# Performance work log

Measured on AMD Instinct MI355X. Metric: run time of the kernel, lower is better.

## Reference

```python
import jax, jax.numpy as jnp
import numpy as np

ATTN_DIM = 512
LEN_DIM = 2048
HEAD = 8
RANK = 8
A_H = ATTN_DIM // HEAD      # 64
L_R = LEN_DIM // RANK       # 256
BS = 32


def setup_inputs() -> dict:
    key = jax.random.key(0)
    ks = jax.random.split(key, 8)
    s = 1.0 / np.sqrt(ATTN_DIM)
    return {
        "x": jax.random.normal(ks[0], (BS, LEN_DIM, ATTN_DIM), dtype=jnp.float32),
        "Wq": jax.random.normal(ks[1], (ATTN_DIM, ATTN_DIM), dtype=jnp.float32) * s,
        "bq": jax.random.normal(ks[2], (ATTN_DIM,), dtype=jnp.float32) * s,
        "Wk": jax.random.normal(ks[3], (ATTN_DIM, ATTN_DIM), dtype=jnp.float32) * s,
        "bk": jax.random.normal(ks[4], (ATTN_DIM,), dtype=jnp.float32) * s,
        "Wv": jax.random.normal(ks[5], (ATTN_DIM, ATTN_DIM), dtype=jnp.float32) * s,
        "bv": jax.random.normal(ks[6], (ATTN_DIM,), dtype=jnp.float32) * s,
        # xavier_normal-ish init for factor [1, a_h, l_r, rank]
        "factor": jax.random.normal(ks[7], (1, A_H, L_R, RANK), dtype=jnp.float32)
        * np.float32(np.sqrt(2.0 / (L_R + RANK))),
    }


def reference(x, Wq, bq, Wk, bk, Wv, bv, factor):
    bs = x.shape[0]
    hr = HEAD * RANK  # 64
    # projections (torch Linear: x @ W.T + b), then view to [bs, a_h, head*rank, l_r]
    q = (jnp.einsum("bld,ed->ble", x, Wq) + bq).reshape(bs, A_H, hr, L_R)
    k = (jnp.einsum("bld,ed->ble", x, Wk) + bk).reshape(bs, A_H, hr, L_R)
    v = (jnp.einsum("bld,ed->ble", x, Wv) + bv).reshape(bs, A_H, hr, L_R)
    f = factor[0]  # [a_h, l_r, rank]
    k = jnp.einsum("bahl,alr->bahr", k, f)  # [bs, a_h, hr, rank]
    v = jnp.einsum("bahl,alr->bahr", v, f)  # [bs, a_h, hr, rank]
    # scores = q^T @ k / sqrt(head*rank): [bs, a_h, l_r, rank]
    scores = jnp.einsum("bahl,bahr->balr", q, k) / jnp.sqrt(jnp.float32(hr))
    attn = jax.nn.softmax(scores, axis=-1)
    # attn @ v^T: [bs, a_h, l_r, hr]
    out = jnp.einsum("balr,bahr->balh", attn, v)
    return out.reshape(bs, LEN_DIM, ATTN_DIM)
```

## Files before the change

kernel.cpp:

```cpp
#include <hip/hip_runtime.h>
#include <hip/hip_bf16.h>
#include <stdint.h>


typedef unsigned short ushort_t;

using bf16x8 = __attribute__((ext_vector_type(8))) short;
using f32x4  = __attribute__((ext_vector_type(4))) float;

__device__ __forceinline__ float bf2f(unsigned short u) {
  union { unsigned int i; float f; } v;
  v.i = ((unsigned int)u) << 16;
  return v.f;
}
__device__ __forceinline__ unsigned short f2bf(float f) {
  __hip_bfloat16 h = __float2bfloat16(f);
  return *reinterpret_cast<unsigned short*>(&h);
}

__device__ __forceinline__ void load_lds16(const void* g, void* l) {
  __builtin_amdgcn_global_load_lds(
      (const __attribute__((address_space(1))) unsigned int*)g,
      (__attribute__((address_space(3))) unsigned int*)l,
      16, 0, 0);
}

__global__ __launch_bounds__(256)
void cast_f32_bf16(const float* __restrict__ src, ushort_t* __restrict__ dst,
                   int n4) {
  int i = blockIdx.x * blockDim.x + threadIdx.x;
  if (i < n4) {
    float4 v = ((const float4*)src)[i];
    ushort_t p[4] = {f2bf(v.x), f2bf(v.y), f2bf(v.z), f2bf(v.w)};
    *(uint2*)(dst + 4 * (size_t)i) = *(const uint2*)p;
  }
}

__global__ __launch_bounds__(256)
void wkv2_pre(const float* __restrict__ Wk, const float* __restrict__ bk,
              const float* __restrict__ Wv, const float* __restrict__ bv,
              const float* __restrict__ F,
              ushort_t* __restrict__ Wk2b, ushort_t* __restrict__ Wv2b,
              float* __restrict__ bk2g, float* __restrict__ bv2g) {
  const int a  = blockIdx.x;
  const int kv = blockIdx.y;
  const float* W = kv ? Wv : Wk;
  const float* B = kv ? bv : bk;
  ushort_t* Wo = kv ? Wv2b : Wk2b;
  float* bo = kv ? bv2g : bk2g;
  const int t = threadIdx.x;

  __shared__ float fs[256][8];
  {
    const float* Fp = F + (size_t)a * 2048 + (size_t)t * 8;
    *(float4*)&fs[t][0] = *(const float4*)Fp;
    *(float4*)&fs[t][4] = *(const float4*)(Fp + 4);
  }
  __syncthreads();

  for (int dblk = 0; dblk < 2; ++dblk) {
    const int d = dblk * 256 + t;
    float acc[2][8];
#pragma unroll
    for (int p = 0; p < 2; ++p)
#pragma unroll
      for (int r = 0; r < 8; ++r) acc[p][r] = 0.f;

    for (int lr = 0; lr < 256; ++lr) {
      const float w0 = W[(size_t)lr * 512 + d];
      const float w1 = W[(size_t)(256 + lr) * 512 + d];
      float4 fa = *(const float4*)&fs[lr][0];
      float4 fb = *(const float4*)&fs[lr][4];
      acc[0][0] += w0 * fa.x; acc[0][1] += w0 * fa.y;
      acc[0][2] += w0 * fa.z; acc[0][3] += w0 * fa.w;
      acc[0][4] += w0 * fb.x; acc[0][5] += w0 * fb.y;
      acc[0][6] += w0 * fb.z; acc[0][7] += w0 * fb.w;
      acc[1][0] += w1 * fa.x; acc[1][1] += w1 * fa.y;
      acc[1][2] += w1 * fa.z; acc[1][3] += w1 * fa.w;
      acc[1][4] += w1 * fb.x; acc[1][5] += w1 * fb.y;
      acc[1][6] += w1 * fb.z; acc[1][7] += w1 * fb.w;
    }
#pragma unroll
    for (int p = 0; p < 2; ++p)
#pragma unroll
      for (int r = 0; r < 8; ++r)
        Wo[((size_t)(a * 2 + p) * 8 + r) * 512 + d] = f2bf(acc[p][r]);
  }

  if (t < 16) {
    const int p = t >> 3, r = t & 7;
    float s = 0.f;
    for (int lr = 0; lr < 256; ++lr) s += B[p * 256 + lr] * fs[lr][r];
    bo[a * 16 + t] = s;
  }
}

__global__ __launch_bounds__(256)
void gemm_q(const ushort_t* __restrict__ X, const ushort_t* __restrict__ W,
            const float* __restrict__ Bi, ushort_t* __restrict__ O) {
  __shared__ __align__(16) short sA[128 * 64];
  __shared__ __align__(16) short sB[128 * 64];

  const int fid = blockIdx.x + 4 * blockIdx.y;
  const int swz = (fid & 7) * 256 + (fid >> 3);
  const int by  = swz >> 2;
  const int bx  = swz & 3;

  const int tid  = threadIdx.x;
  const int lane = tid & 63;
  const int wid  = tid >> 6;
  const int m0 = by * 128;
  const int n0 = bx * 128;
  const int wave_m = (wid & 1) * 64;
  const int wave_n = (wid >> 1) * 64;
  const int quad = lane >> 4;
  const int l15  = lane & 15;

  f32x4 acc[4][4];
#pragma unroll
  for (int i = 0; i < 4; ++i)
#pragma unroll
    for (int j = 0; j < 4; ++j) acc[i][j] = f32x4{0.f, 0.f, 0.f, 0.f};

  int srow[4], scol[4];
#pragma unroll
  for (int q = 0; q < 4; ++q) {
    const int c = q * 256 + wid * 64 + lane;
    srow[q] = c >> 3;
    scol[q] = ((c & 7) ^ ((c >> 3) & 7)) * 8;
  }

  for (int kt = 0; kt < 512; kt += 64) {
#pragma unroll
    for (int q = 0; q < 4; ++q) {
      const ushort_t* ga = X + ((size_t)(m0 + srow[q]) << 9) + kt + scol[q];
      const ushort_t* gb = W + ((size_t)(n0 + srow[q]) << 9) + kt + scol[q];
      load_lds16(ga, &sA[(q * 256 + wid * 64) * 8]);
      load_lds16(gb, &sB[(q * 256 + wid * 64) * 8]);
    }
    __syncthreads();

#pragma unroll
    for (int ks = 0; ks < 2; ++ks) {
      bf16x8 af[4], bfr[4];
#pragma unroll
      for (int i = 0; i < 4; ++i) {
        const int row = wave_m + i * 16 + l15;
        af[i] = *(const bf16x8*)&sA[row * 64 + ((ks * 4 + quad) ^ (row & 7)) * 8];
      }
#pragma unroll
      for (int j = 0; j < 4; ++j) {
        const int row = wave_n + j * 16 + l15;
        bfr[j] = *(const bf16x8*)&sB[row * 64 + ((ks * 4 + quad) ^ (row & 7)) * 8];
      }
#pragma unroll
      for (int i = 0; i < 4; ++i)
#pragma unroll
        for (int j = 0; j < 4; ++j)
          acc[i][j] = __builtin_amdgcn_mfma_f32_16x16x32_bf16(af[i], bfr[j],
                                                              acc[i][j], 0, 0, 0);
    }
    __syncthreads();
  }

#pragma unroll
  for (int j = 0; j < 4; ++j) {
    const int gn = n0 + wave_n + j * 16 + l15;
    const float bv = Bi[gn];
#pragma unroll
    for (int i = 0; i < 4; ++i) {
      const int gmBase = m0 + wave_m + i * 16 + quad * 4;
      f32x4 c = acc[i][j];
#pragma unroll
      for (int rg = 0; rg < 4; ++rg) {
        O[((size_t)(gmBase + rg) << 9) + gn] = f2bf(c[rg] + bv);
      }
    }
  }
}

__global__ __launch_bounds__(256)
void k2v2_gemm(const ushort_t* __restrict__ X,
               const ushort_t* __restrict__ Wk2b,
               const ushort_t* __restrict__ Wv2b,
               const float* __restrict__ bk2g, const float* __restrict__ bv2g,
               float* __restrict__ k2g, float* __restrict__ v2g) {
  const int a = blockIdx.x;
  const int b = blockIdx.y;
  __shared__ __align__(16) short sX[32 * 512];
  __shared__ __align__(16) short sW[32 * 512];

  const int t = threadIdx.x;
  const int lane = t & 63;
  const int wid  = t >> 6;

#pragma unroll
  for (int q = 0; q < 8; ++q) {
    const int c = q * 256 + wid * 64 + lane;
    const int row = c >> 6;
    const int sch = (c & 63) ^ (row & 7);
    const ushort_t* gx =
        X + ((size_t)(b * 2048 + a * 32 + row) << 9) + sch * 8;
    const ushort_t* gw =
        (row < 16 ? Wk2b + (size_t)(a * 16 + row) * 512
                  : Wv2b + (size_t)(a * 16 + row - 16) * 512) + sch * 8;
    load_lds16(gx, &sX[(q * 256 + wid * 64) * 8]);
    load_lds16(gw, &sW[(q * 256 + wid * 64) * 8]);
  }
  __syncthreads();

  const int kv = wid >> 1;
  const int mf = wid & 1;
  const int quad = lane >> 4;
  const int l15  = lane & 15;

  f32x4 acc = f32x4{0.f, 0.f, 0.f, 0.f};
  const int arow = mf * 16 + l15;
  const int brow = kv * 16 + l15;
#pragma unroll
  for (int ks = 0; ks < 16; ++ks) {
    bf16x8 af =
        *(const bf16x8*)&sX[arow * 512 + (((ks * 4 + quad) ^ (arow & 7))) * 8];
    bf16x8 bf_ =
        *(const bf16x8*)&sW[brow * 512 + (((ks * 4 + quad) ^ (brow & 7))) * 8];
    acc = __builtin_amdgcn_mfma_f32_16x16x32_bf16(af, bf_, acc, 0, 0, 0);
  }

  const float* bb = kv ? bv2g : bk2g;
  float* og = kv ? v2g : k2g;
  const float bias = bb[a * 16 + l15];
  const size_t obase = ((size_t)(b * 64 + a)) * 512;
#pragma unroll
  for (int rg = 0; rg < 4; ++rg) {
    const int lh = mf * 16 + quad * 4 + rg;
    const int h = 2 * lh + (l15 >> 3);
    const int r = l15 & 7;
    og[obase + h * 8 + r] = acc[rg] + bias;
  }
}

__global__ __launch_bounds__(256)
void attn_pv(const ushort_t* __restrict__ Q, const float* __restrict__ k2g,
             const float* __restrict__ v2g, float* __restrict__ Out) {
  const int a = blockIdx.x;
  const int b = blockIdx.y;
  const int t = threadIdx.x;

  __shared__ float k2[64][8];
  __shared__ float v2T[8][64];
  __shared__ float pl[256][8];

  {
    const size_t base = ((size_t)b * 64 + a) * 512;
    if (t < 64) {
      float4 x0 = *(const float4*)(k2g + base + t * 8);
      float4 x1 = *(const float4*)(k2g + base + t * 8 + 4);
      *(float4*)&k2[t][0] = x0;
      *(float4*)&k2[t][4] = x1;
    } else if (t < 128) {
      const int h = t - 64;
      float4 v0 = *(const float4*)(v2g + base + h * 8);
      float4 v1 = *(const float4*)(v2g + base + h * 8 + 4);
      v2T[0][h] = v0.x; v2T[1][h] = v0.y; v2T[2][h] = v0.z; v2T[3][h] = v0.w;
      v2T[4][h] = v1.x; v2T[5][h] = v1.y; v2T[6][h] = v1.z; v2T[7][h] = v1.w;
    }
  }
  __syncthreads();

  {
    const int lr = t;
    float s[8];
#pragma unroll
    for (int r = 0; r < 8; ++r) s[r] = 0.f;

    const ushort_t* Qp = Q + (((size_t)(b * 2048 + a * 32)) << 9) + lr;
#pragma unroll 16
    for (int h = 0; h < 64; ++h) {
      const float qv = bf2f(Qp[(size_t)h * 256]);
      float4 ka = *(const float4*)&k2[h][0];
      float4 kb = *(const float4*)&k2[h][4];
      s[0] += qv * ka.x; s[1] += qv * ka.y; s[2] += qv * ka.z; s[3] += qv * ka.w;
      s[4] += qv * kb.x; s[5] += qv * kb.y; s[6] += qv * kb.z; s[7] += qv * kb.w;
    }

    float mx = -1e30f;
#pragma unroll
    for (int r = 0; r < 8; ++r) { s[r] *= 0.125f; mx = fmaxf(mx, s[r]); }
    float sum = 0.f;
#pragma unroll
    for (int r = 0; r < 8; ++r) { s[r] = __expf(s[r] - mx); sum += s[r]; }
    const float inv = 1.0f / sum;
    *(float4*)&pl[lr][0] = float4{s[0] * inv, s[1] * inv, s[2] * inv, s[3] * inv};
    *(float4*)&pl[lr][4] = float4{s[4] * inv, s[5] * inv, s[6] * inv, s[7] * inv};
  }
  __syncthreads();

  {
    float* Ob = Out + (((size_t)(b * 2048 + a * 32)) << 9);
    const int g  = (t >> 4) & 7;
    const int h0 = (t & 15) * 4;
#pragma unroll
    for (int iter = 0; iter < 16; ++iter) {
      const int row = (t >> 7) + iter * 2;
      const int lr = row * 8 + g;
      float p[8];
      *(float4*)&p[0] = *(const float4*)&pl[lr][0];
      *(float4*)&p[4] = *(const float4*)&pl[lr][4];
      float4 o = float4{0.f, 0.f, 0.f, 0.f};
#pragma unroll
      for (int r = 0; r < 8; ++r) {
        float4 vt = *(const float4*)&v2T[r][h0];
        o.x += p[r] * vt.x; o.y += p[r] * vt.y;
        o.z += p[r] * vt.z; o.w += p[r] * vt.w;
      }
      *(float4*)(Ob + (size_t)row * 512 + g * 64 + h0) = o;
    }
  }
}

extern "C" void kernel_launch(void* const* d_in, const int* in_sizes, int n_in,
                              void* d_out, int out_size, void* d_ws,
                              size_t ws_size, hipStream_t stream) {
  const float* x  = (const float*)d_in[0];
  const float* Wq = (const float*)d_in[1];
  const float* bq = (const float*)d_in[2];
  const float* Wk = (const float*)d_in[3];
  const float* bk = (const float*)d_in[4];
  const float* Wv = (const float*)d_in[5];
  const float* bv = (const float*)d_in[6];
  const float* f  = (const float*)d_in[7];
  float* out = (float*)d_out;

  ushort_t* xb   = (ushort_t*)d_ws;
  ushort_t* wqb  = xb + 33554432u;
  ushort_t* Qb   = wqb + 262144u;
  ushort_t* Wk2b = Qb + 33554432u;
  ushort_t* Wv2b = Wk2b + 524288u;
  float* k2g  = (float*)(Wv2b + 524288u);
  float* v2g  = k2g + 1048576u;
  float* bk2g = v2g + 1048576u;
  float* bv2g = bk2g + 1024u;

  cast_f32_bf16<<<32768, 256, 0, stream>>>(x, xb, 8388608);
  cast_f32_bf16<<<256, 256, 0, stream>>>(Wq, wqb, 65536);

  dim3 gp(64, 2);
  wkv2_pre<<<gp, 256, 0, stream>>>(Wk, bk, Wv, bv, f, Wk2b, Wv2b, bk2g, bv2g);

  dim3 g1(4, 512);
  gemm_q<<<g1, 256, 0, stream>>>(xb, wqb, bq, Qb);

  dim3 g2(64, 32);
  k2v2_gemm<<<g2, 256, 0, stream>>>(xb, Wk2b, Wv2b, bk2g, bv2g, k2g, v2g);
  attn_pv<<<g2, 256, 0, stream>>>(Qb, k2g, v2g, out);
}
```

Baseline: 401.1 us.

## Fold K factor into x to eliminate Q projection GEMM and intermediates

Reassociates the scores computation: each (batch, a) block computes G = x_slice^T · k2 from fp32 x, which it casts in-kernel, so scores become Wq2 · G plus a bias correction. This removes the full Q projection GEMM, the bf16 copy of x, and the Q round trip through global memory. The cost is a 1024-deep scores GEMM per block pair that rereads the reorganised Wq from cache, and G is rounded to bf16, which changes numerical error. wkv2_pre is also split across an extra grid dimension for more parallelism.

```diff
diff --git a/kernel.cpp b/kernel.cpp
--- a/kernel.cpp
+++ b/kernel.cpp
@@ -26,14 +26,15 @@
 }
 
 __global__ __launch_bounds__(256)
-void cast_f32_bf16(const float* __restrict__ src, ushort_t* __restrict__ dst,
-                   int n4) {
-  int i = blockIdx.x * blockDim.x + threadIdx.x;
-  if (i < n4) {
-    float4 v = ((const float4*)src)[i];
-    ushort_t p[4] = {f2bf(v.x), f2bf(v.y), f2bf(v.z), f2bf(v.w)};
-    *(uint2*)(dst + 4 * (size_t)i) = *(const uint2*)p;
-  }
+void cast_wq2(const float* __restrict__ Wq, ushort_t* __restrict__ Wq2b) {
+  const int i = blockIdx.x * 256 + threadIdx.x;
+  float4 v = ((const float4*)Wq)[i];
+  const int row = i >> 7;
+  const int c4  = i & 127;
+  const int lr = row & 255;
+  const int p  = row >> 8;
+  ushort_t pk[4] = {f2bf(v.x), f2bf(v.y), f2bf(v.z), f2bf(v.w)};
+  *(uint2*)(Wq2b + (size_t)lr * 1024 + p * 512 + c4 * 4) = *(const uint2*)pk;
 }
 
 __global__ __launch_bounds__(256)
@@ -42,8 +43,9 @@
               const float* __restrict__ F,
               ushort_t* __restrict__ Wk2b, ushort_t* __restrict__ Wv2b,
               float* __restrict__ bk2g, float* __restrict__ bv2g) {
-  const int a  = blockIdx.x;
-  const int kv = blockIdx.y;
+  const int a    = blockIdx.x;
+  const int kv   = blockIdx.y;
+  const int dblk = blockIdx.z;
   const float* W = kv ? Wv : Wk;
   const float* B = kv ? bv : bk;
   ushort_t* Wo = kv ? Wv2b : Wk2b;
@@ -58,36 +60,35 @@
   }
   __syncthreads();
 
-  for (int dblk = 0; dblk < 2; ++dblk) {
-    const int d = dblk * 256 + t;
-    float acc[2][8];
-#pragma unroll
-    for (int p = 0; p < 2; ++p)
-#pragma unroll
-      for (int r = 0; r < 8; ++r) acc[p][r] = 0.f;
-
-    for (int lr = 0; lr < 256; ++lr) {
-      const float w0 = W[(size_t)lr * 512 + d];
-      const float w1 = W[(size_t)(256 + lr) * 512 + d];
-      float4 fa = *(const float4*)&fs[lr][0];
-      float4 fb = *(const float4*)&fs[lr][4];
-      acc[0][0] += w0 * fa.x; acc[0][1] += w0 * fa.y;
-      acc[0][2] += w0 * fa.z; acc[0][3] += w0 * fa.w;
-      acc[0][4] += w0 * fb.x; acc[0][5] += w0 * fb.y;
-      acc[0][6] += w0 * fb.z; acc[0][7] += w0 * fb.w;
-      acc[1][0] += w1 * fa.x; acc[1][1] += w1 * fa.y;
-      acc[1][2] += w1 * fa.z; acc[1][3] += w1 * fa.w;
-      acc[1][4] += w1 * fb.x; acc[1][5] += w1 * fb.y;
-      acc[1][6] += w1 * fb.z; acc[1][7] += w1 * fb.w;
-    }
-#pragma unroll
-    for (int p = 0; p < 2; ++p)
-#pragma unroll
-      for (int r = 0; r < 8; ++r)
-        Wo[((size_t)(a * 2 + p) * 8 + r) * 512 + d] = f2bf(acc[p][r]);
-  }
-
-  if (t < 16) {
+  const int d = dblk * 256 + t;
+  float acc[2][8];
+#pragma unroll
+  for (int p = 0; p < 2; ++p)
+#pragma unroll
+    for (int r = 0; r < 8; ++r) acc[p][r] = 0.f;
+
+#pragma unroll 4
+  for (int lr = 0; lr < 256; ++lr) {
+    const float w0 = W[(size_t)lr * 512 + d];
+    const float w1 = W[(size_t)(256 + lr) * 512 + d];
+    float4 fa = *(const float4*)&fs[lr][0];
+    float4 fb = *(const float4*)&fs[lr][4];
+    acc[0][0] += w0 * fa.x; acc[0][1] += w0 * fa.y;
+    acc[0][2] += w0 * fa.z; acc[0][3] += w0 * fa.w;
+    acc[0][4] += w0 * fb.x; acc[0][5] += w0 * fb.y;
+    acc[0][6] += w0 * fb.z; acc[0][7] += w0 * fb.w;
+    acc[1][0] += w1 * fa.x; acc[1][1] += w1 * fa.y;
+    acc[1][2] += w1 * fa.z; acc[1][3] += w1 * fa.w;
+    acc[1][4] += w1 * fb.x; acc[1][5] += w1 * fb.y;
+    acc[1][6] += w1 * fb.z; acc[1][7] += w1 * fb.w;
+  }
+#pragma unroll
+  for (int p = 0; p < 2; ++p)
+#pragma unroll
+    for (int r = 0; r < 8; ++r)
+      Wo[(size_t)(a * 16 + p * 8 + r) * 512 + d] = f2bf(acc[p][r]);
+
+  if (dblk == 0 && t < 16) {
     const int p = t >> 3, r = t & 7;
     float s = 0.f;
     for (int lr = 0; lr < 256; ++lr) s += B[p * 256 + lr] * fs[lr][r];
@@ -96,224 +97,238 @@
 }
 
 __global__ __launch_bounds__(256)
-void gemm_q(const ushort_t* __restrict__ X, const ushort_t* __restrict__ W,
-            const float* __restrict__ Bi, ushort_t* __restrict__ O) {
-  __shared__ __align__(16) short sA[128 * 64];
-  __shared__ __align__(16) short sB[128 * 64];
-
-  const int fid = blockIdx.x + 4 * blockIdx.y;
-  const int swz = (fid & 7) * 256 + (fid >> 3);
-  const int by  = swz >> 2;
-  const int bx  = swz & 3;
-
-  const int tid  = threadIdx.x;
-  const int lane = tid & 63;
-  const int wid  = tid >> 6;
-  const int m0 = by * 128;
-  const int n0 = bx * 128;
-  const int wave_m = (wid & 1) * 64;
-  const int wave_n = (wid >> 1) * 64;
-  const int quad = lane >> 4;
-  const int l15  = lane & 15;
-
-  f32x4 acc[4][4];
-#pragma unroll
-  for (int i = 0; i < 4; ++i)
-#pragma unroll
-    for (int j = 0; j < 4; ++j) acc[i][j] = f32x4{0.f, 0.f, 0.f, 0.f};
-
-  int srow[4], scol[4];
-#pragma unroll
-  for (int q = 0; q < 4; ++q) {
-    const int c = q * 256 + wid * 64 + lane;
-    srow[q] = c >> 3;
-    scol[q] = ((c & 7) ^ ((c >> 3) & 7)) * 8;
-  }
-
-  for (int kt = 0; kt < 512; kt += 64) {
-#pragma unroll
-    for (int q = 0; q < 4; ++q) {
-      const ushort_t* ga = X + ((size_t)(m0 + srow[q]) << 9) + kt + scol[q];
-      const ushort_t* gb = W + ((size_t)(n0 + srow[q]) << 9) + kt + scol[q];
-      load_lds16(ga, &sA[(q * 256 + wid * 64) * 8]);
-      load_lds16(gb, &sB[(q * 256 + wid * 64) * 8]);
-    }
-    __syncthreads();
-
-#pragma unroll
-    for (int ks = 0; ks < 2; ++ks) {
-      bf16x8 af[4], bfr[4];
-#pragma unroll
-      for (int i = 0; i < 4; ++i) {
-        const int row = wave_m + i * 16 + l15;
-        af[i] = *(const bf16x8*)&sA[row * 64 + ((ks * 4 + quad) ^ (row & 7)) * 8];
-      }
-#pragma unroll
-      for (int j = 0; j < 4; ++j) {
-        const int row = wave_n + j * 16 + l15;
-        bfr[j] = *(const bf16x8*)&sB[row * 64 + ((ks * 4 + quad) ^ (row & 7)) * 8];
-      }
-#pragma unroll
-      for (int i = 0; i < 4; ++i)
-#pragma unroll
-        for (int j = 0; j < 4; ++j)
-          acc[i][j] = __builtin_amdgcn_mfma_f32_16x16x32_bf16(af[i], bfr[j],
-                                                              acc[i][j], 0, 0, 0);
-    }
-    __syncthreads();
-  }
-
-#pragma unroll
-  for (int j = 0; j < 4; ++j) {
-    const int gn = n0 + wave_n + j * 16 + l15;
-    const float bv = Bi[gn];
-#pragma unroll
-    for (int i = 0; i < 4; ++i) {
-      const int gmBase = m0 + wave_m + i * 16 + quad * 4;
-      f32x4 c = acc[i][j];
-#pragma unroll
-      for (int rg = 0; rg < 4; ++rg) {
-        O[((size_t)(gmBase + rg) << 9) + gn] = f2bf(c[rg] + bv);
-      }
-    }
-  }
-}
-
-__global__ __launch_bounds__(256)
-void k2v2_gemm(const ushort_t* __restrict__ X,
-               const ushort_t* __restrict__ Wk2b,
-               const ushort_t* __restrict__ Wv2b,
-               const float* __restrict__ bk2g, const float* __restrict__ bv2g,
-               float* __restrict__ k2g, float* __restrict__ v2g) {
+void xfold(const float* __restrict__ X,
+           const ushort_t* __restrict__ Wk2b, const ushort_t* __restrict__ Wv2b,
+           const float* __restrict__ bk2g, const float* __restrict__ bv2g,
+           ushort_t* __restrict__ Gb, float* __restrict__ v2g,
+           float* __restrict__ skg) {
   const int a = blockIdx.x;
   const int b = blockIdx.y;
+  const int t = threadIdx.x;
+  const int lane = t & 63, wid = t >> 6;
+  const int quad = lane >> 4, l15 = lane & 15;
+  const int ba = b * 64 + a;
+
   __shared__ __align__(16) short sX[32 * 512];
   __shared__ __align__(16) short sW[32 * 512];
-
-  const int t = threadIdx.x;
-  const int lane = t & 63;
-  const int wid  = t >> 6;
+  __shared__ float k2s[64][8];
 
 #pragma unroll
   for (int q = 0; q < 8; ++q) {
     const int c = q * 256 + wid * 64 + lane;
     const int row = c >> 6;
     const int sch = (c & 63) ^ (row & 7);
-    const ushort_t* gx =
-        X + ((size_t)(b * 2048 + a * 32 + row) << 9) + sch * 8;
     const ushort_t* gw =
         (row < 16 ? Wk2b + (size_t)(a * 16 + row) * 512
                   : Wv2b + (size_t)(a * 16 + row - 16) * 512) + sch * 8;
-    load_lds16(gx, &sX[(q * 256 + wid * 64) * 8]);
     load_lds16(gw, &sW[(q * 256 + wid * 64) * 8]);
+  }
+#pragma unroll
+  for (int q = 0; q < 8; ++q) {
+    const int c = q * 256 + t;
+    const int lh = c >> 6, ch = c & 63;
+    const float* gx = X + ((size_t)(b * 2048 + a * 32 + lh) << 9) + ch * 8;
+    float4 x0 = *(const float4*)gx;
+    float4 x1 = *(const float4*)(gx + 4);
+    ushort_t pk[8] = {f2bf(x0.x), f2bf(x0.y), f2bf(x0.z), f2bf(x0.w),
+                      f2bf(x1.x), f2bf(x1.y), f2bf(x1.z), f2bf(x1.w)};
+    *(bf16x8*)&sX[lh * 512 + ((ch ^ (lh & 7)) << 3)] = *(const bf16x8*)pk;
   }
   __syncthreads();
 
   const int kv = wid >> 1;
   const int mf = wid & 1;
-  const int quad = lane >> 4;
-  const int l15  = lane & 15;
-
   f32x4 acc = f32x4{0.f, 0.f, 0.f, 0.f};
   const int arow = mf * 16 + l15;
   const int brow = kv * 16 + l15;
 #pragma unroll
   for (int ks = 0; ks < 16; ++ks) {
-    bf16x8 af =
-        *(const bf16x8*)&sX[arow * 512 + (((ks * 4 + quad) ^ (arow & 7))) * 8];
-    bf16x8 bf_ =
-        *(const bf16x8*)&sW[brow * 512 + (((ks * 4 + quad) ^ (brow & 7))) * 8];
+    bf16x8 af  = *(const bf16x8*)&sX[arow * 512 + ((ks * 4 + quad) ^ (arow & 7)) * 8];
+    bf16x8 bf_ = *(const bf16x8*)&sW[brow * 512 + ((ks * 4 + quad) ^ (brow & 7)) * 8];
     acc = __builtin_amdgcn_mfma_f32_16x16x32_bf16(af, bf_, acc, 0, 0, 0);
   }
-
-  const float* bb = kv ? bv2g : bk2g;
-  float* og = kv ? v2g : k2g;
-  const float bias = bb[a * 16 + l15];
-  const size_t obase = ((size_t)(b * 64 + a)) * 512;
-#pragma unroll
-  for (int rg = 0; rg < 4; ++rg) {
-    const int lh = mf * 16 + quad * 4 + rg;
-    const int h = 2 * lh + (l15 >> 3);
-    const int r = l15 & 7;
-    og[obase + h * 8 + r] = acc[rg] + bias;
+  const float bias = (kv ? bv2g : bk2g)[a * 16 + l15];
+  if (kv == 0) {
+#pragma unroll
+    for (int rg = 0; rg < 4; ++rg) {
+      const int lh = mf * 16 + quad * 4 + rg;
+      k2s[2 * lh + (l15 >> 3)][l15 & 7] = acc[rg] + bias;
+    }
+  } else {
+    const size_t obase = (size_t)ba * 512;
+#pragma unroll
+    for (int rg = 0; rg < 4; ++rg) {
+      const int lh = mf * 16 + quad * 4 + rg;
+      const int h = 2 * lh + (l15 >> 3);
+      v2g[obase + h * 8 + (l15 & 7)] = acc[rg] + bias;
+    }
+  }
+  __syncthreads();
+
+  if (t < 16) {
+    const int p = t >> 3, r = t & 7;
+    float s = 0.f;
+#pragma unroll
+    for (int lh = 0; lh < 32; ++lh) s += k2s[2 * lh + p][r];
+    skg[ba * 16 + t] = s;
+  }
+  {
+    const int p  = t >> 7;
+    const int d0 = (t & 127) * 4;
+    float g[4][8];
+#pragma unroll
+    for (int dd = 0; dd < 4; ++dd)
+#pragma unroll
+      for (int r = 0; r < 8; ++r) g[dd][r] = 0.f;
+
+#pragma unroll
+    for (int lh = 0; lh < 32; ++lh) {
+      float kr[8];
+      *(float4*)&kr[0] = *(const float4*)&k2s[2 * lh + p][0];
+      *(float4*)&kr[4] = *(const float4*)&k2s[2 * lh + p][4];
+      const int ch = d0 >> 3;
+      uint2 xr = *(const uint2*)&sX[lh * 512 + ((ch ^ (lh & 7)) << 3) + (d0 & 7)];
+      const ushort_t* xs = (const ushort_t*)&xr;
+      float xv[4] = {bf2f(xs[0]), bf2f(xs[1]), bf2f(xs[2]), bf2f(xs[3])};
+#pragma unroll
+      for (int dd = 0; dd < 4; ++dd)
+#pragma unroll
+        for (int r = 0; r < 8; ++r) g[dd][r] += xv[dd] * kr[r];
+    }
+#pragma unroll
+    for (int r = 0; r < 8; ++r) {
+      ushort_t pk[4] = {f2bf(g[0][r]), f2bf(g[1][r]), f2bf(g[2][r]),
+                        f2bf(g[3][r])};
+      *(uint2*)(Gb + (((size_t)(ba * 8 + r)) << 10) + p * 512 + d0) =
+          *(const uint2*)pk;
+    }
   }
 }
 
 __global__ __launch_bounds__(256)
-void attn_pv(const ushort_t* __restrict__ Q, const float* __restrict__ k2g,
-             const float* __restrict__ v2g, float* __restrict__ Out) {
-  const int a = blockIdx.x;
-  const int b = blockIdx.y;
+void scores_pv(const ushort_t* __restrict__ Wq2b, const ushort_t* __restrict__ Gb,
+               const float* __restrict__ bq, const float* __restrict__ skg,
+               const float* __restrict__ v2g, float* __restrict__ Out) {
+  const int P = blockIdx.x;
   const int t = threadIdx.x;
-
-  __shared__ float k2[64][8];
-  __shared__ float v2T[8][64];
-  __shared__ float pl[256][8];
-
-  {
-    const size_t base = ((size_t)b * 64 + a) * 512;
-    if (t < 64) {
-      float4 x0 = *(const float4*)(k2g + base + t * 8);
-      float4 x1 = *(const float4*)(k2g + base + t * 8 + 4);
-      *(float4*)&k2[t][0] = x0;
-      *(float4*)&k2[t][4] = x1;
-    } else if (t < 128) {
-      const int h = t - 64;
-      float4 v0 = *(const float4*)(v2g + base + h * 8);
-      float4 v1 = *(const float4*)(v2g + base + h * 8 + 4);
-      v2T[0][h] = v0.x; v2T[1][h] = v0.y; v2T[2][h] = v0.z; v2T[3][h] = v0.w;
-      v2T[4][h] = v1.x; v2T[5][h] = v1.y; v2T[6][h] = v1.z; v2T[7][h] = v1.w;
-    }
-  }
+  const int lane = t & 63, wid = t >> 6;
+  const int quad = lane >> 4, l15 = lane & 15;
+
+  __shared__ __align__(16) short sA[256 * 64];
+  __shared__ __align__(16) short sB[16 * 64];
+  __shared__ float sS[256 * 16];
+  __shared__ float v2T[2][8][64];
+  __shared__ float sks[32];
+
+  if (t < 128) {
+    const int pa = t >> 6, h = t & 63;
+    const float* vp = v2g + (size_t)(2 * P + pa) * 512 + h * 8;
+    float4 v0 = *(const float4*)vp;
+    float4 v1 = *(const float4*)(vp + 4);
+    v2T[pa][0][h] = v0.x; v2T[pa][1][h] = v0.y;
+    v2T[pa][2][h] = v0.z; v2T[pa][3][h] = v0.w;
+    v2T[pa][4][h] = v1.x; v2T[pa][5][h] = v1.y;
+    v2T[pa][6][h] = v1.z; v2T[pa][7][h] = v1.w;
+  }
+  if (t < 32) sks[t] = skg[P * 32 + t];
+
+  f32x4 acc[4];
+#pragma unroll
+  for (int i = 0; i < 4; ++i) acc[i] = f32x4{0.f, 0.f, 0.f, 0.f};
+
+  const int wave_m = wid * 64;
+  const int grow0 = P * 16;
+
+  for (int kt = 0; kt < 1024; kt += 64) {
+#pragma unroll
+    for (int q = 0; q < 8; ++q) {
+      const int c = q * 256 + wid * 64 + lane;
+      const int row = c >> 3, ch = c & 7;
+      load_lds16(Wq2b + (size_t)row * 1024 + kt + ((ch ^ (row & 7)) << 3),
+                 &sA[(q * 256 + wid * 64) * 8]);
+    }
+    if (wid < 2) {
+      const int c = wid * 64 + lane;
+      const int row = c >> 3, ch = c & 7;
+      load_lds16(Gb + (size_t)(grow0 + row) * 1024 + kt + ((ch ^ (row & 7)) << 3),
+                 &sB[(wid * 64) * 8]);
+    }
+    __syncthreads();
+#pragma unroll
+    for (int ks = 0; ks < 2; ++ks) {
+      bf16x8 bfrag =
+          *(const bf16x8*)&sB[l15 * 64 + (((ks * 4 + quad) ^ (l15 & 7)) << 3)];
+#pragma unroll
+      for (int i = 0; i < 4; ++i) {
+        const int row = wave_m + i * 16 + l15;
+        bf16x8 afrag =
+            *(const bf16x8*)&sA[row * 64 + (((ks * 4 + quad) ^ (row & 7)) << 3)];
+        acc[i] = __builtin_amdgcn_mfma_f32_16x16x32_bf16(afrag, bfrag, acc[i],
+                                                         0, 0, 0);
+      }
+    }
+    __syncthreads();
+  }
+
+#pragma unroll
+  for (int i = 0; i < 4; ++i)
+#pragma unroll
+    for (int rg = 0; rg < 4; ++rg)
+      sS[(wave_m + i * 16 + quad * 4 + rg) * 16 + l15] = acc[i][rg];
   __syncthreads();
 
   {
     const int lr = t;
-    float s[8];
-#pragma unroll
-    for (int r = 0; r < 8; ++r) s[r] = 0.f;
-
-    const ushort_t* Qp = Q + (((size_t)(b * 2048 + a * 32)) << 9) + lr;
-#pragma unroll 16
-    for (int h = 0; h < 64; ++h) {
-      const float qv = bf2f(Qp[(size_t)h * 256]);
-      float4 ka = *(const float4*)&k2[h][0];
-      float4 kb = *(const float4*)&k2[h][4];
-      s[0] += qv * ka.x; s[1] += qv * ka.y; s[2] += qv * ka.z; s[3] += qv * ka.w;
-      s[4] += qv * kb.x; s[5] += qv * kb.y; s[6] += qv * kb.z; s[7] += qv * kb.w;
-    }
-
-    float mx = -1e30f;
-#pragma unroll
-    for (int r = 0; r < 8; ++r) { s[r] *= 0.125f; mx = fmaxf(mx, s[r]); }
-    float sum = 0.f;
-#pragma unroll
-    for (int r = 0; r < 8; ++r) { s[r] = __expf(s[r] - mx); sum += s[r]; }
-    const float inv = 1.0f / sum;
-    *(float4*)&pl[lr][0] = float4{s[0] * inv, s[1] * inv, s[2] * inv, s[3] * inv};
-    *(float4*)&pl[lr][4] = float4{s[4] * inv, s[5] * inv, s[6] * inv, s[7] * inv};
+    const float bq0 = bq[lr];
+    const float bq1 = bq[256 + lr];
+#pragma unroll
+    for (int pa = 0; pa < 2; ++pa) {
+      float s[8];
+      *(float4*)&s[0] = *(const float4*)&sS[lr * 16 + pa * 8];
+      *(float4*)&s[4] = *(const float4*)&sS[lr * 16 + pa * 8 + 4];
+      float mx = -1e30f;
+#pragma unroll
+      for (int r = 0; r < 8; ++r) {
+        s[r] = (s[r] + bq0 * sks[pa * 16 + r] + bq1 * sks[pa * 16 + 8 + r]) *
+               0.125f;
+        mx = fmaxf(mx, s[r]);
+      }
+      float sum = 0.f;
+#pragma unroll
+      for (int r = 0; r < 8; ++r) { s[r] = __expf(s[r] - mx); sum += s[r]; }
+      const float inv = 1.0f / sum;
+      *(float4*)&sS[lr * 16 + pa * 8] =
+          float4{s[0] * inv, s[1] * inv, s[2] * inv, s[3] * inv};
+      *(float4*)&sS[lr * 16 + pa * 8 + 4] =
+          float4{s[4] * inv, s[5] * inv, s[6] * inv, s[7] * inv};
+    }
   }
   __syncthreads();
 
   {
-    float* Ob = Out + (((size_t)(b * 2048 + a * 32)) << 9);
-    const int g  = (t >> 4) & 7;
+    const int b  = (2 * P) >> 6;
+    const int a0 = (2 * P) & 63;
+    const int g0 = (t >> 4) & 7;
     const int h0 = (t & 15) * 4;
 #pragma unroll
-    for (int iter = 0; iter < 16; ++iter) {
-      const int row = (t >> 7) + iter * 2;
-      const int lr = row * 8 + g;
-      float p[8];
-      *(float4*)&p[0] = *(const float4*)&pl[lr][0];
-      *(float4*)&p[4] = *(const float4*)&pl[lr][4];
-      float4 o = float4{0.f, 0.f, 0.f, 0.f};
-#pragma unroll
-      for (int r = 0; r < 8; ++r) {
-        float4 vt = *(const float4*)&v2T[r][h0];
-        o.x += p[r] * vt.x; o.y += p[r] * vt.y;
-        o.z += p[r] * vt.z; o.w += p[r] * vt.w;
+    for (int pa = 0; pa < 2; ++pa) {
+      float* Ob = Out + (((size_t)(b * 2048 + (a0 + pa) * 32)) << 9);
+#pragma unroll
+      for (int iter = 0; iter < 16; ++iter) {
+        const int row = (t >> 7) + iter * 2;
+        const int lr = row * 8 + g0;
+        float p[8];
+        *(float4*)&p[0] = *(const float4*)&sS[lr * 16 + pa * 8];
+        *(float4*)&p[4] = *(const float4*)&sS[lr * 16 + pa * 8 + 4];
+        float4 o = float4{0.f, 0.f, 0.f, 0.f};
+#pragma unroll
+        for (int r = 0; r < 8; ++r) {
+          float4 vt = *(const float4*)&v2T[pa][r][h0];
+          o.x += p[r] * vt.x; o.y += p[r] * vt.y;
+          o.z += p[r] * vt.z; o.w += p[r] * vt.w;
+        }
+        *(float4*)(Ob + (size_t)row * 512 + g0 * 64 + h0) = o;
       }
-      *(float4*)(Ob + (size_t)row * 512 + g * 64 + h0) = o;
     }
   }
 }
@@ -331,26 +346,22 @@
   const float* f  = (const float*)d_in[7];
   float* out = (float*)d_out;
 
-  ushort_t* xb   = (ushort_t*)d_ws;
-  ushort_t* wqb  = xb + 33554432u;
-  ushort_t* Qb   = wqb + 262144u;
-  ushort_t* Wk2b = Qb + 33554432u;
+  ushort_t* Wq2b = (ushort_t*)d_ws;
+  ushort_t* Wk2b = Wq2b + 262144u;
   ushort_t* Wv2b = Wk2b + 524288u;
-  float* k2g  = (float*)(Wv2b + 524288u);
-  float* v2g  = k2g + 1048576u;
+  ushort_t* Gb   = Wv2b + 524288u;
+  float* v2g  = (float*)(Gb + 16777216u);
   float* bk2g = v2g + 1048576u;
   float* bv2g = bk2g + 1024u;
-
-  cast_f32_bf16<<<32768, 256, 0, stream>>>(x, xb, 8388608);
-  cast_f32_bf16<<<256, 256, 0, stream>>>(Wq, wqb, 65536);
-
-  dim3 gp(64, 2);
+  float* skg  = bv2g + 1024u;
+
+  cast_wq2<<<256, 256, 0, stream>>>(Wq, Wq2b);
+
+  dim3 gp(64, 2, 2);
   wkv2_pre<<<gp, 256, 0, stream>>>(Wk, bk, Wv, bv, f, Wk2b, Wv2b, bk2g, bv2g);
 
-  dim3 g1(4, 512);
-  gemm_q<<<g1, 256, 0, stream>>>(xb, wqb, bq, Qb);
-
-  dim3 g2(64, 32);
-  k2v2_gemm<<<g2, 256, 0, stream>>>(xb, Wk2b, Wv2b, bk2g, bv2g, k2g, v2g);
-  attn_pv<<<g2, 256, 0, stream>>>(Qb, k2g, v2g, out);
-}
+  dim3 gx(64, 32);
+  xfold<<<gx, 256, 0, stream>>>(x, Wk2b, Wv2b, bk2g, bv2g, Gb, v2g, skg);
+
+  scores_pv<<<1024, 256, 0, stream>>>(Wq2b, Gb, bq, skg, v2g, out);
+}
```

New measurement: 326.0 us. -18.7%, faster.
